# Kernel optimization log

Hardware: AMD Instinct MI355X
Metric: run time of the kernel (lower is better)

The kernel has to match this reference:

```python
import jax, jax.numpy as jnp
import numpy as np

BATCH, FIELD0, EMB = 1024, 32, 64
LAYER_SIZES = (128, 128, 128)  # split_half=True -> hidden field sizes [32, 64, 64]


def setup_inputs() -> dict:
    key = jax.random.key(0)
    ks = jax.random.split(key, 7)
    x = jax.random.normal(ks[0], (BATCH, FIELD0, EMB), dtype=jnp.float32)
    # Conv1D(kernel_size=1) weights: (in_channels=f0*fi, filters=layer_size), plus bias.
    field_sizes = [FIELD0]
    params = {}
    for i, size in enumerate(LAYER_SIZES):
        fi = field_sizes[-1]
        fan_in = FIELD0 * fi
        scale = 1.0 / np.sqrt(fan_in)
        params[f"W{i}"] = jax.random.normal(ks[1 + 2 * i], (fan_in, size), dtype=jnp.float32) * scale
        params[f"b{i}"] = jnp.zeros((size,), dtype=jnp.float32)
        field_sizes.append(size // 2 if i != len(LAYER_SIZES) - 1 else size)
    return {"x": x, **params}


def reference(x, W0, b0, W1, b1, W2, b2):
    # CIN: outer product + 1x1 conv (a matmul over the flattened field-pair axis)
    # fused as a single bilinear contraction per layer:
    #   cur[b,k,e] = sum_{i,j} x[b,i,e] * hidden[b,j,e] * W[i,j,k] + b[k]
    Ws = [(W0, b0), (W1, b1), (W2, b2)]
    f0 = x.shape[1]
    hidden = x
    final_outputs = []
    n_layers = len(Ws)
    for idx, (W, b) in enumerate(Ws):
        fi = hidden.shape[1]
        Wr = W.reshape(f0, fi, W.shape[-1])  # channel m = i*fi + j (row-major reshape)
        cur = jnp.einsum('bie,bje,ijk->bke', x, hidden, Wr) + b[None, :, None]
        # activation=None -> linear
        if idx != n_layers - 1:
            half = cur.shape[1] // 2
            hidden, direct = cur[:, :half, :], cur[:, half:, :]
        else:
            direct = cur
        final_outputs.append(direct)
    result = jnp.concatenate(final_outputs, axis=1)  # (B, 64+64+128, E)
    return jnp.sum(result, axis=-1)  # (B, 256)
```

## Files before the change

### kernel.cpp

```cpp
#include <hip/hip_runtime.h>
#include <cstdint>


typedef _Float16 half8  __attribute__((ext_vector_type(8)));
typedef _Float16 half4_ __attribute__((ext_vector_type(4)));
typedef _Float16 half2_ __attribute__((ext_vector_type(2)));
typedef float    f32x4  __attribute__((ext_vector_type(4)));

__global__ void pack_w_all(const float* __restrict__ W0, _Float16* __restrict__ Wt0,
                           const float* __restrict__ W1, _Float16* __restrict__ Wt1,
                           const float* __restrict__ W2, _Float16* __restrict__ Wt2)
{
    __shared__ _Float16 ldsT[128 * 33];
    const int blk = blockIdx.x, t = threadIdx.x;
    const float* W;
    _Float16* Wt;
    int c;
    if (blk < 32)       { W = W0; Wt = Wt0; c = blk; }
    else if (blk < 96)  { W = W1; Wt = Wt1; c = blk - 32; }
    else                { W = W2; Wt = Wt2; c = blk - 96; }

    for (int p = t; p < 32 * 128; p += 256) {
        int kk = p >> 7, m = p & 127;
        ldsT[m * 33 + kk] = (_Float16)W[(size_t)(c * 32 + kk) * 128 + m];
    }
    __syncthreads();
    int m = t >> 1, kk0 = (t & 1) * 16;
    half8 v0, v1;
#pragma unroll
    for (int i = 0; i < 8; ++i) {
        v0[i] = ldsT[m * 33 + kk0 + i];
        v1[i] = ldsT[m * 33 + kk0 + 8 + i];
    }
    *(half8*)(Wt + (size_t)c * 4096 + t * 16)     = v0;
    *(half8*)(Wt + (size_t)c * 4096 + t * 16 + 8) = v1;
}

__global__ __launch_bounds__(128, 4)
void cin_fused(const float* __restrict__ x,
               const _Float16* __restrict__ Wt0,
               const _Float16* __restrict__ Wt1,
               const float* __restrict__ bs0,
               const float* __restrict__ bs1,
               _Float16* __restrict__ S0,
               _Float16* __restrict__ S1,
               _Float16* __restrict__ S2)
{
    __shared__ alignas(16) char smem[22528];
    _Float16* sX  = (_Float16*)smem;
    _Float16* R_A = (_Float16*)(smem + 4096);
    _Float16* R_B = (_Float16*)(smem + 13312);

    const int t = threadIdx.x, lane = t & 63, ks = t >> 6;
    const int lr = lane & 15, q = lane >> 4;
    const int b = blockIdx.x;

    {
        const float4* xv = (const float4*)(x + (size_t)b * 2048);
#pragma unroll
        for (int s = 0; s < 4; ++s) {
            int p4 = t + s * 128;
            float4 v = xv[p4];
            int idx = p4 * 4, i = idx >> 6, e0 = idx & 63;
            _Float16 h0 = (_Float16)v.x, h1 = (_Float16)v.y;
            _Float16 h2 = (_Float16)v.z, h3 = (_Float16)v.w;
            half4_ pk = {h0, h1, h2, h3};
            *(half4_*)(sX + i * 64 + e0) = pk;
            *(half4_*)(R_B + i * 72 + e0) = pk;
            R_A[(e0 + 0) * 40 + i] = h0;
            R_A[(e0 + 1) * 40 + i] = h1;
            R_A[(e0 + 2) * 40 + i] = h2;
            R_A[(e0 + 3) * 40 + i] = h3;
        }
    }
    __syncthreads();

    const half8 aF0 = *(const half8*)(R_B + (ks * 16 + lr) * 72 + q * 8);
    const half8 aF1 = *(const half8*)(R_B + (ks * 16 + lr) * 72 + q * 8 + 32);

    f32x4 acc[2][4];

    auto kloop = [&](const _Float16* WtL, int nch, int ish,
                     const _Float16* hb, int ph) {
#pragma unroll
        for (int mt = 0; mt < 2; ++mt)
#pragma unroll
            for (int nt = 0; nt < 4; ++nt)
                acc[mt][nt] = f32x4{0.0f, 0.0f, 0.0f, 0.0f};
        const _Float16* aG = WtL + (ks * 32 + lr) * 32 + q * 8;
        const _Float16* hP = hb + lr * ph + q * 8;
        const _Float16* xP = sX + lr;
        half8 afA[2], afB[2], hvA[4], hvB[4];
        _Float16 xsA[4], xsB[4];
        auto pf = [&](half8* af, half8* hv, _Float16* xs, int c) {
            const int i  = c >> ish;
            const int j0 = (c - (i << ish)) << 5;
            const _Float16* ag = aG + (size_t)c * 4096;
            af[0] = *(const half8*)(ag);
            af[1] = *(const half8*)(ag + 512);
#pragma unroll
            for (int nt = 0; nt < 4; ++nt) {
                hv[nt] = *(const half8*)(hP + nt * (ph << 4) + j0);
                xs[nt] = xP[(i << 6) + (nt << 4)];
            }
        };
        auto cp = [&](half8* af, half8* hv, _Float16* xs) {
#pragma unroll
            for (int nt = 0; nt < 4; ++nt) {
                half2_ xv2 = {xs[nt], xs[nt]};
                half8 xv8 = __builtin_shufflevector(xv2, xv2, 0, 1, 0, 1, 0, 1, 0, 1);
                half8 bf = hv[nt] * xv8;
                acc[0][nt] = __builtin_amdgcn_mfma_f32_16x16x32_f16(
                    af[0], bf, acc[0][nt], 0, 0, 0);
                acc[1][nt] = __builtin_amdgcn_mfma_f32_16x16x32_f16(
                    af[1], bf, acc[1][nt], 0, 0, 0);
            }
        };
        pf(afA, hvA, xsA, 0);
        for (int c = 0; c < nch; c += 2) {
            pf(afB, hvB, xsB, c + 1);
            cp(afA, hvA, xsA);
            if (c + 2 < nch) pf(afA, hvA, xsA, c + 2);
            cp(afB, hvB, xsB);
        }
    };

    auto sgemm = [&](const _Float16* hJ, int fi, _Float16* Sdst) {
        const int njt = fi >> 4;
        for (int jt = 0; jt < njt; ++jt) {
            f32x4 sa = {0.0f, 0.0f, 0.0f, 0.0f};
            half8 bv0 = *(const half8*)(hJ + (jt * 16 + lr) * 72 + q * 8);
            half8 bv1 = *(const half8*)(hJ + (jt * 16 + lr) * 72 + q * 8 + 32);
            sa = __builtin_amdgcn_mfma_f32_16x16x32_f16(aF0, bv0, sa, 0, 0, 0);
            sa = __builtin_amdgcn_mfma_f32_16x16x32_f16(aF1, bv1, sa, 0, 0, 0);
#pragma unroll
            for (int r = 0; r < 4; ++r)
                Sdst[(size_t)b * (32 * fi) + (ks * 16 + q * 4 + r) * fi
                     + jt * 16 + lr] = (_Float16)sa[r];
        }
    };

    auto epi = [&](const float* bs, _Float16* hJ, _Float16* hT, bool wantT) {
#pragma unroll
        for (int mt = 0; mt < 2; ++mt) {
            const int jb = ks * 32 + mt * 16 + q * 4;
            const float b0f = bs[jb + 0], b1f = bs[jb + 1];
            const float b2f = bs[jb + 2], b3f = bs[jb + 3];
#pragma unroll
            for (int nt = 0; nt < 4; ++nt) {
                const int e = nt * 16 + lr;
                half4_ vh;
                vh[0] = (_Float16)(acc[mt][nt][0] + b0f);
                vh[1] = (_Float16)(acc[mt][nt][1] + b1f);
                vh[2] = (_Float16)(acc[mt][nt][2] + b2f);
                vh[3] = (_Float16)(acc[mt][nt][3] + b3f);
                hJ[(jb + 0) * 72 + e] = vh[0];
                hJ[(jb + 1) * 72 + e] = vh[1];
                hJ[(jb + 2) * 72 + e] = vh[2];
                hJ[(jb + 3) * 72 + e] = vh[3];
                if (wantT) *(half4_*)(hT + e * 72 + jb) = vh;
            }
        }
    };

    sgemm(R_B, 32, S0);
    kloop(Wt0, 32, 0, R_A, 40);
    __syncthreads();
    epi(bs0, R_A, R_B, true);
    __syncthreads();
    sgemm(R_A, 64, S1);
    kloop(Wt1, 64, 1, R_B, 72);
    __syncthreads();
    epi(bs1, R_B, nullptr, false);
    __syncthreads();
    sgemm(R_B, 64, S2);
}

__global__ __launch_bounds__(256, 2)
void cin_direct(const _Float16* __restrict__ S0v, const _Float16* __restrict__ S1v,
                const _Float16* __restrict__ S2v,
                const _Float16* __restrict__ Wt0, const _Float16* __restrict__ Wt1,
                const _Float16* __restrict__ Wt2,
                const float* __restrict__ bs0, const float* __restrict__ bs1,
                const float* __restrict__ bs2,
                float* __restrict__ out)
{
    __shared__ f32x4 red[2][64];
    const int t = threadIdx.x, lane = t & 63, w = t >> 6;
    const int lr = lane & 15, q = lane >> 4;
    const int task = blockIdx.x * 2 + (w >> 1);
    const int kh = w & 1;

    const _Float16 *S, *Wt;
    const float* bias;
    int fan, nch, dm0, ob, idx;
    if (task < 256)      { S = S0v; Wt = Wt0; bias = bs0; fan = 1024; nch = 32; dm0 = 64; ob = 0;   idx = task; }
    else if (task < 512) { S = S1v; Wt = Wt1; bias = bs1; fan = 2048; nch = 64; dm0 = 64; ob = 64;  idx = task - 256; }
    else                 { S = S2v; Wt = Wt2; bias = bs2; fan = 2048; nch = 64; dm0 = 0;  ob = 128; idx = task - 512; }
    const int bt = idx & 63, kt = idx >> 6;
    const int bbase = bt * 16;
    const int hn = nch >> 1, c0 = kh * hn;

    const _Float16* aG = Wt + (size_t)(dm0 + kt * 16 + lr) * 32 + q * 8
                            + (size_t)c0 * 4096;
    const _Float16* bG = S + (size_t)(bbase + lr) * fan + q * 8 + c0 * 32;

    f32x4 acc = {0.0f, 0.0f, 0.0f, 0.0f};
    half8 aA = *(const half8*)(aG);
    half8 bA = *(const half8*)(bG);
    for (int c = 0; c < hn; c += 2) {
        half8 aB = *(const half8*)(aG + (size_t)(c + 1) * 4096);
        half8 bB = *(const half8*)(bG + (c + 1) * 32);
        acc = __builtin_amdgcn_mfma_f32_16x16x32_f16(aA, bA, acc, 0, 0, 0);
        if (c + 2 < hn) {
            aA = *(const half8*)(aG + (size_t)(c + 2) * 4096);
            bA = *(const half8*)(bG + (c + 2) * 32);
        }
        acc = __builtin_amdgcn_mfma_f32_16x16x32_f16(aB, bB, acc, 0, 0, 0);
    }
    if (kh == 1) red[w >> 1][lane] = acc;
    __syncthreads();
    if (kh == 0) {
        f32x4 o = red[w >> 1][lane];
#pragma unroll
        for (int r = 0; r < 4; ++r) {
            int kl = kt * 16 + q * 4 + r;
            out[(size_t)(bbase + lr) * 256 + ob + kl]
                = acc[r] + o[r] + 64.0f * bias[dm0 + kl];
        }
    }
}

extern "C" void kernel_launch(void* const* d_in, const int* in_sizes, int n_in,
                              void* d_out, int out_size, void* d_ws, size_t ws_size,
                              hipStream_t stream)
{
    const float* x  = (const float*)d_in[0];
    const float* W0 = (const float*)d_in[1];
    const float* b0 = (const float*)d_in[2];
    const float* W1 = (const float*)d_in[3];
    const float* b1 = (const float*)d_in[4];
    const float* W2 = (const float*)d_in[5];
    const float* b2 = (const float*)d_in[6];
    float* out = (float*)d_out;

    char* ws = (char*)d_ws;
    _Float16* Wt0 = (_Float16*)(ws + 0);
    _Float16* Wt1 = (_Float16*)(ws + 262144);
    _Float16* Wt2 = (_Float16*)(ws + 786432);
    _Float16* S0  = (_Float16*)(ws + 1310720);
    _Float16* S1  = (_Float16*)(ws + 3407872);
    _Float16* S2  = (_Float16*)(ws + 7602176);
    (void)in_sizes; (void)n_in; (void)out_size; (void)ws_size;

    hipLaunchKernelGGL(pack_w_all, dim3(160), dim3(256), 0, stream,
                       W0, Wt0, W1, Wt1, W2, Wt2);

    hipLaunchKernelGGL(cin_fused, dim3(1024), dim3(128), 0, stream,
                       x, Wt0, Wt1, b0, b1, S0, S1, S2);

    hipLaunchKernelGGL(cin_direct, dim3(512), dim3(256), 0, stream,
                       S0, S1, S2, Wt0, Wt1, Wt2, b0, b1, b2, out);
}
```

Before: 116.4 us.

## Split cin_fused work across four waves instead of two per block

Doubles the cin_fused block from 128 to 256 threads. Each of the four waves now owns a 16-row slice of the 64 output channels, with one A-fragment and four accumulators instead of two and eight. The small S-GEMM tiles are spread round-robin over the waves. This aims to raise wave-level parallelism and cut per-thread register pressure, at the cost of each wave redundantly loading the H/x operands and holding more waves per block.

```diff
diff --git a/kernel.cpp b/kernel.cpp
--- a/kernel.cpp
+++ b/kernel.cpp
@@ -36,7 +36,7 @@
     *(half8*)(Wt + (size_t)c * 4096 + t * 16 + 8) = v1;
 }
 
-__global__ __launch_bounds__(128, 4)
+__global__ __launch_bounds__(256, 4)
 void cin_fused(const float* __restrict__ x,
                const _Float16* __restrict__ Wt0,
                const _Float16* __restrict__ Wt1,
@@ -51,15 +51,15 @@
     _Float16* R_A = (_Float16*)(smem + 4096);
     _Float16* R_B = (_Float16*)(smem + 13312);
 
-    const int t = threadIdx.x, lane = t & 63, ks = t >> 6;
+    const int t = threadIdx.x, lane = t & 63, w = t >> 6;
     const int lr = lane & 15, q = lane >> 4;
     const int b = blockIdx.x;
 
     {
         const float4* xv = (const float4*)(x + (size_t)b * 2048);
 #pragma unroll
-        for (int s = 0; s < 4; ++s) {
-            int p4 = t + s * 128;
+        for (int s = 0; s < 2; ++s) {
+            int p4 = t + s * 256;
             float4 v = xv[p4];
             int idx = p4 * 4, i = idx >> 6, e0 = idx & 63;
             _Float16 h0 = (_Float16)v.x, h1 = (_Float16)v.y;
@@ -75,45 +75,43 @@
     }
     __syncthreads();
 
-    const half8 aF0 = *(const half8*)(R_B + (ks * 16 + lr) * 72 + q * 8);
-    const half8 aF1 = *(const half8*)(R_B + (ks * 16 + lr) * 72 + q * 8 + 32);
-
-    f32x4 acc[2][4];
+    half8 aF[2][2];
+#pragma unroll
+    for (int it = 0; it < 2; ++it) {
+        aF[it][0] = *(const half8*)(R_B + (it * 16 + lr) * 72 + q * 8);
+        aF[it][1] = *(const half8*)(R_B + (it * 16 + lr) * 72 + q * 8 + 32);
+    }
+
+    f32x4 acc[4];
 
     auto kloop = [&](const _Float16* WtL, int nch, int ish,
                      const _Float16* hb, int ph) {
 #pragma unroll
-        for (int mt = 0; mt < 2; ++mt)
-#pragma unroll
-            for (int nt = 0; nt < 4; ++nt)
-                acc[mt][nt] = f32x4{0.0f, 0.0f, 0.0f, 0.0f};
-        const _Float16* aG = WtL + (ks * 32 + lr) * 32 + q * 8;
+        for (int nt = 0; nt < 4; ++nt)
+            acc[nt] = f32x4{0.0f, 0.0f, 0.0f, 0.0f};
+        const _Float16* aG = WtL + (w * 16 + lr) * 32 + q * 8;
         const _Float16* hP = hb + lr * ph + q * 8;
         const _Float16* xP = sX + lr;
-        half8 afA[2], afB[2], hvA[4], hvB[4];
+        half8 afA, afB, hvA[4], hvB[4];
         _Float16 xsA[4], xsB[4];
-        auto pf = [&](half8* af, half8* hv, _Float16* xs, int c) {
+        auto pf = [&](half8& af, half8* hv, _Float16* xs, int c) {
             const int i  = c >> ish;
             const int j0 = (c - (i << ish)) << 5;
-            const _Float16* ag = aG + (size_t)c * 4096;
-            af[0] = *(const half8*)(ag);
-            af[1] = *(const half8*)(ag + 512);
+            af = *(const half8*)(aG + (size_t)c * 4096);
 #pragma unroll
             for (int nt = 0; nt < 4; ++nt) {
                 hv[nt] = *(const half8*)(hP + nt * (ph << 4) + j0);
                 xs[nt] = xP[(i << 6) + (nt << 4)];
             }
         };
-        auto cp = [&](half8* af, half8* hv, _Float16* xs) {
+        auto cp = [&](half8& af, half8* hv, _Float16* xs) {
 #pragma unroll
             for (int nt = 0; nt < 4; ++nt) {
                 half2_ xv2 = {xs[nt], xs[nt]};
                 half8 xv8 = __builtin_shufflevector(xv2, xv2, 0, 1, 0, 1, 0, 1, 0, 1);
                 half8 bf = hv[nt] * xv8;
-                acc[0][nt] = __builtin_amdgcn_mfma_f32_16x16x32_f16(
-                    af[0], bf, acc[0][nt], 0, 0, 0);
-                acc[1][nt] = __builtin_amdgcn_mfma_f32_16x16x32_f16(
-                    af[1], bf, acc[1][nt], 0, 0, 0);
+                acc[nt] = __builtin_amdgcn_mfma_f32_16x16x32_f16(
+                    af, bf, acc[nt], 0, 0, 0);
             }
         };
         pf(afA, hvA, xsA, 0);
@@ -126,40 +124,38 @@
     };
 
     auto sgemm = [&](const _Float16* hJ, int fi, _Float16* Sdst) {
-        const int njt = fi >> 4;
-        for (int jt = 0; jt < njt; ++jt) {
+        const int nT = fi >> 3;
+        for (int tt = w; tt < nT; tt += 4) {
+            const int it = tt & 1, jt = tt >> 1;
             f32x4 sa = {0.0f, 0.0f, 0.0f, 0.0f};
             half8 bv0 = *(const half8*)(hJ + (jt * 16 + lr) * 72 + q * 8);
             half8 bv1 = *(const half8*)(hJ + (jt * 16 + lr) * 72 + q * 8 + 32);
-            sa = __builtin_amdgcn_mfma_f32_16x16x32_f16(aF0, bv0, sa, 0, 0, 0);
-            sa = __builtin_amdgcn_mfma_f32_16x16x32_f16(aF1, bv1, sa, 0, 0, 0);
+            sa = __builtin_amdgcn_mfma_f32_16x16x32_f16(aF[it][0], bv0, sa, 0, 0, 0);
+            sa = __builtin_amdgcn_mfma_f32_16x16x32_f16(aF[it][1], bv1, sa, 0, 0, 0);
 #pragma unroll
             for (int r = 0; r < 4; ++r)
-                Sdst[(size_t)b * (32 * fi) + (ks * 16 + q * 4 + r) * fi
+                Sdst[(size_t)b * (32 * fi) + (it * 16 + q * 4 + r) * fi
                      + jt * 16 + lr] = (_Float16)sa[r];
         }
     };
 
     auto epi = [&](const float* bs, _Float16* hJ, _Float16* hT, bool wantT) {
-#pragma unroll
-        for (int mt = 0; mt < 2; ++mt) {
-            const int jb = ks * 32 + mt * 16 + q * 4;
-            const float b0f = bs[jb + 0], b1f = bs[jb + 1];
-            const float b2f = bs[jb + 2], b3f = bs[jb + 3];
-#pragma unroll
-            for (int nt = 0; nt < 4; ++nt) {
-                const int e = nt * 16 + lr;
-                half4_ vh;
-                vh[0] = (_Float16)(acc[mt][nt][0] + b0f);
-                vh[1] = (_Float16)(acc[mt][nt][1] + b1f);
-                vh[2] = (_Float16)(acc[mt][nt][2] + b2f);
-                vh[3] = (_Float16)(acc[mt][nt][3] + b3f);
-                hJ[(jb + 0) * 72 + e] = vh[0];
-                hJ[(jb + 1) * 72 + e] = vh[1];
-                hJ[(jb + 2) * 72 + e] = vh[2];
-                hJ[(jb + 3) * 72 + e] = vh[3];
-                if (wantT) *(half4_*)(hT + e * 72 + jb) = vh;
-            }
+        const int jb = w * 16 + q * 4;
+        const float b0f = bs[jb + 0], b1f = bs[jb + 1];
+        const float b2f = bs[jb + 2], b3f = bs[jb + 3];
+#pragma unroll
+        for (int nt = 0; nt < 4; ++nt) {
+            const int e = nt * 16 + lr;
+            half4_ vh;
+            vh[0] = (_Float16)(acc[nt][0] + b0f);
+            vh[1] = (_Float16)(acc[nt][1] + b1f);
+            vh[2] = (_Float16)(acc[nt][2] + b2f);
+            vh[3] = (_Float16)(acc[nt][3] + b3f);
+            hJ[(jb + 0) * 72 + e] = vh[0];
+            hJ[(jb + 1) * 72 + e] = vh[1];
+            hJ[(jb + 2) * 72 + e] = vh[2];
+            hJ[(jb + 3) * 72 + e] = vh[3];
+            if (wantT) *(half4_*)(hT + e * 72 + jb) = vh;
         }
     };
 
@@ -256,7 +252,7 @@
     hipLaunchKernelGGL(pack_w_all, dim3(160), dim3(256), 0, stream,
                        W0, Wt0, W1, Wt1, W2, Wt2);
 
-    hipLaunchKernelGGL(cin_fused, dim3(1024), dim3(128), 0, stream,
+    hipLaunchKernelGGL(cin_fused, dim3(1024), dim3(256), 0, stream,
                        x, Wt0, Wt1, b0, b1, S0, S1, S2);
 
     hipLaunchKernelGGL(cin_direct, dim3(512), dim3(256), 0, stream,
```

New measurement: 137.6 us. 18.2% more time.

## Split CIN k-loop across waves by channel with LDS partial-sum exchange

Applied to the files above, without the earlier changes.

Each of the two waves now computes all 64 output rows over half of the input channel chunks, instead of 32 rows over all chunks. Partial accumulators are exchanged through a new LDS region and summed before the epilogue. This halves each wave's k-loop length and raises A-fragment reuse per loaded B fragment. The cost is doubled accumulator registers, more LDS (lower occupancy, launch bounds reduced to 2) and an extra exchange step with a barrier.

```diff
diff --git a/kernel.cpp b/kernel.cpp
--- a/kernel.cpp
+++ b/kernel.cpp
@@ -36,7 +36,65 @@
     *(half8*)(Wt + (size_t)c * 4096 + t * 16 + 8) = v1;
 }
 
-__global__ __launch_bounds__(128, 4)
+template<int NCH, int ISH, int PH>
+__device__ __forceinline__ void kloop_t(f32x4 (&acc)[4][4],
+    const _Float16* __restrict__ WtL, const _Float16* __restrict__ hb,
+    const _Float16* __restrict__ sX, int lr, int q, int ks)
+{
+#pragma unroll
+    for (int mt = 0; mt < 4; ++mt)
+#pragma unroll
+        for (int nt = 0; nt < 4; ++nt)
+            acc[mt][nt] = f32x4{0.0f, 0.0f, 0.0f, 0.0f};
+
+    constexpr int HC = NCH / 2;
+    const int c0 = ks * HC;
+    const _Float16* aG = WtL + (size_t)c0 * 4096 + lr * 32 + q * 8;
+    const _Float16* hP = hb + lr * PH + q * 8;
+    const _Float16* xP = sX + lr;
+
+    half8 afA[4], afB[4], hvA[4], hvB[4];
+    _Float16 xsA[4], xsB[4];
+
+    auto pf = [&](half8* af, half8* hv, _Float16* xs, int cc) {
+        const int c  = c0 + cc;
+        const int i  = c >> ISH;
+        const int j0 = (c & ((1 << ISH) - 1)) << 5;
+        const _Float16* ag = aG + (size_t)cc * 4096;
+#pragma unroll
+        for (int mt = 0; mt < 4; ++mt)
+            af[mt] = *(const half8*)(ag + mt * 512);
+        const _Float16* hh = hP + j0;
+        const _Float16* xb = xP + (i << 6);
+#pragma unroll
+        for (int nt = 0; nt < 4; ++nt) {
+            hv[nt] = *(const half8*)(hh + nt * (PH * 16));
+            xs[nt] = xb[nt * 16];
+        }
+    };
+    auto cp = [&](half8* af, half8* hv, _Float16* xs) {
+#pragma unroll
+        for (int nt = 0; nt < 4; ++nt) {
+            half2_ xv2 = {xs[nt], xs[nt]};
+            half8 xv8 = __builtin_shufflevector(xv2, xv2, 0, 1, 0, 1, 0, 1, 0, 1);
+            half8 bf = hv[nt] * xv8;
+#pragma unroll
+            for (int mt = 0; mt < 4; ++mt)
+                acc[mt][nt] = __builtin_amdgcn_mfma_f32_16x16x32_f16(
+                    af[mt], bf, acc[mt][nt], 0, 0, 0);
+        }
+    };
+
+    pf(afA, hvA, xsA, 0);
+    for (int cc = 0; cc < HC; cc += 2) {
+        pf(afB, hvB, xsB, cc + 1);
+        cp(afA, hvA, xsA);
+        if (cc + 2 < HC) pf(afA, hvA, xsA, cc + 2);
+        cp(afB, hvB, xsB);
+    }
+}
+
+__global__ __launch_bounds__(128, 2)
 void cin_fused(const float* __restrict__ x,
                const _Float16* __restrict__ Wt0,
                const _Float16* __restrict__ Wt1,
@@ -46,10 +104,11 @@
                _Float16* __restrict__ S1,
                _Float16* __restrict__ S2)
 {
-    __shared__ alignas(16) char smem[22528];
+    __shared__ alignas(16) char smem[38912];
     _Float16* sX  = (_Float16*)smem;
     _Float16* R_A = (_Float16*)(smem + 4096);
     _Float16* R_B = (_Float16*)(smem + 13312);
+    f32x4*    XC  = (f32x4*)   (smem + 22528);
 
     const int t = threadIdx.x, lane = t & 63, ks = t >> 6;
     const int lr = lane & 15, q = lane >> 4;
@@ -78,51 +137,25 @@
     const half8 aF0 = *(const half8*)(R_B + (ks * 16 + lr) * 72 + q * 8);
     const half8 aF1 = *(const half8*)(R_B + (ks * 16 + lr) * 72 + q * 8 + 32);
 
-    f32x4 acc[2][4];
-
-    auto kloop = [&](const _Float16* WtL, int nch, int ish,
-                     const _Float16* hb, int ph) {
-#pragma unroll
-        for (int mt = 0; mt < 2; ++mt)
+    f32x4 acc[4][4];
+
+    auto xchg_write = [&]() {
+        const int om = (1 - ks) * 2;
+#pragma unroll
+        for (int mt2 = 0; mt2 < 2; ++mt2)
 #pragma unroll
             for (int nt = 0; nt < 4; ++nt)
-                acc[mt][nt] = f32x4{0.0f, 0.0f, 0.0f, 0.0f};
-        const _Float16* aG = WtL + (ks * 32 + lr) * 32 + q * 8;
-        const _Float16* hP = hb + lr * ph + q * 8;
-        const _Float16* xP = sX + lr;
-        half8 afA[2], afB[2], hvA[4], hvB[4];
-        _Float16 xsA[4], xsB[4];
-        auto pf = [&](half8* af, half8* hv, _Float16* xs, int c) {
-            const int i  = c >> ish;
-            const int j0 = (c - (i << ish)) << 5;
-            const _Float16* ag = aG + (size_t)c * 4096;
-            af[0] = *(const half8*)(ag);
-            af[1] = *(const half8*)(ag + 512);
+                XC[ks * 512 + (mt2 * 4 + nt) * 64 + lane] = acc[om + mt2][nt];
+    };
+    auto xchg_read = [&]() {
+        const int sm = ks * 2;
+#pragma unroll
+        for (int mt2 = 0; mt2 < 2; ++mt2)
 #pragma unroll
             for (int nt = 0; nt < 4; ++nt) {
-                hv[nt] = *(const half8*)(hP + nt * (ph << 4) + j0);
-                xs[nt] = xP[(i << 6) + (nt << 4)];
+                f32x4 p = XC[(1 - ks) * 512 + (mt2 * 4 + nt) * 64 + lane];
+                acc[sm + mt2][nt] += p;
             }
-        };
-        auto cp = [&](half8* af, half8* hv, _Float16* xs) {
-#pragma unroll
-            for (int nt = 0; nt < 4; ++nt) {
-                half2_ xv2 = {xs[nt], xs[nt]};
-                half8 xv8 = __builtin_shufflevector(xv2, xv2, 0, 1, 0, 1, 0, 1, 0, 1);
-                half8 bf = hv[nt] * xv8;
-                acc[0][nt] = __builtin_amdgcn_mfma_f32_16x16x32_f16(
-                    af[0], bf, acc[0][nt], 0, 0, 0);
-                acc[1][nt] = __builtin_amdgcn_mfma_f32_16x16x32_f16(
-                    af[1], bf, acc[1][nt], 0, 0, 0);
-            }
-        };
-        pf(afA, hvA, xsA, 0);
-        for (int c = 0; c < nch; c += 2) {
-            pf(afB, hvB, xsB, c + 1);
-            cp(afA, hvA, xsA);
-            if (c + 2 < nch) pf(afA, hvA, xsA, c + 2);
-            cp(afB, hvB, xsB);
-        }
     };
 
     auto sgemm = [&](const _Float16* hJ, int fi, _Float16* Sdst) {
@@ -142,8 +175,9 @@
 
     auto epi = [&](const float* bs, _Float16* hJ, _Float16* hT, bool wantT) {
 #pragma unroll
-        for (int mt = 0; mt < 2; ++mt) {
-            const int jb = ks * 32 + mt * 16 + q * 4;
+        for (int mt2 = 0; mt2 < 2; ++mt2) {
+            const int mt = ks * 2 + mt2;
+            const int jb = ks * 32 + mt2 * 16 + q * 4;
             const float b0f = bs[jb + 0], b1f = bs[jb + 1];
             const float b2f = bs[jb + 2], b3f = bs[jb + 3];
 #pragma unroll
@@ -164,13 +198,17 @@
     };
 
     sgemm(R_B, 32, S0);
-    kloop(Wt0, 32, 0, R_A, 40);
-    __syncthreads();
+    kloop_t<32, 0, 40>(acc, Wt0, R_A, sX, lr, q, ks);
+    xchg_write();
+    __syncthreads();
+    xchg_read();
     epi(bs0, R_A, R_B, true);
     __syncthreads();
     sgemm(R_A, 64, S1);
-    kloop(Wt1, 64, 1, R_B, 72);
-    __syncthreads();
+    kloop_t<64, 1, 72>(acc, Wt1, R_B, sX, lr, q, ks);
+    xchg_write();
+    __syncthreads();
+    xchg_read();
     epi(bs1, R_B, nullptr, false);
     __syncthreads();
     sgemm(R_B, 64, S2);
```

Result: slower. 137.2 us (+17.9%).
